# Kernel tuning notes

Measured on AMD Instinct MI355X. Metric: run time of the kernel, lower is better.

Reference implementation:

```python
import jax, jax.numpy as jnp
import numpy as np
import math

B, H, N, L = 8, 512, 64, 2048


def setup_inputs() -> dict:
    key = jax.random.key(0)
    k_u, k_c, k_dt, k_d, k_w, k_b, k_ar, k_ai = jax.random.split(key, 8)
    u = jax.random.normal(k_u, (B, H, L), dtype=jnp.float32)
    # C ~ complex randn, stored as (..., 2) real/imag pairs (torch.view_as_real)
    C_ri = jax.random.normal(k_c, (H, N, 2), dtype=jnp.float32)
    # log_dt ~ Uniform(log(dt_min), log(dt_max))
    lo, hi = math.log(0.001), math.log(0.1)
    log_dt = jax.random.uniform(k_dt, (H,), dtype=jnp.float32) * (hi - lo) + lo
    D = jax.random.normal(k_d, (H,), dtype=jnp.float32)
    # Conv1d(H, 2H, kernel_size=1) -> weight (2H, H), bias (2H), kaiming-ish scale
    W = jax.random.normal(k_w, (2 * H, H), dtype=jnp.float32) / math.sqrt(H)
    b = jax.random.normal(k_b, (2 * H,), dtype=jnp.float32) * 0.01
    # Fixed diagonal state matrix A: Re(A) uniform in [-0.9, -0.8), Im(A) random
    a_re = -0.9 + 0.1 * jax.random.uniform(k_ar, (N,), dtype=jnp.float32)
    a_im = math.pi * jnp.arange(N, dtype=jnp.float32)  # stable oscillation freqs
    A_ri = jnp.stack([a_re, a_im], axis=-1)
    return {"u": u, "C_ri": C_ri, "log_dt": log_dt, "D": D, "W": W, "b": b, "A_ri": A_ri}


def _forward(u, C_ri, log_dt, D, W, b, A_ri):
    Lseq = u.shape[-1]
    C = C_ri[..., 0] + 1j * C_ri[..., 1]          # (H, N) complex
    A = A_ri[..., 0] + 1j * A_ri[..., 1]          # (N,) complex
    dt = jnp.exp(log_dt)                           # (H,)
    dtA = dt[:, None] * A[None, :]                 # (H, N)
    # Vandermonde: exp(dtA * l) for l in [0, L)  -> (H, N, L) complex
    K = jnp.exp(dtA[:, :, None] * jnp.arange(Lseq, dtype=jnp.float32))
    Ct = C * (jnp.exp(dtA) - 1.0) / A              # (H, N)
    k = 2.0 * jnp.einsum('hn,hnl->hl', Ct, K).real  # (H, L) real kernel
    # FFT long convolution (linear conv via length-2L circular conv)
    nfft = 2 * Lseq
    y = jnp.fft.irfft(jnp.fft.rfft(u, n=nfft) * jnp.fft.rfft(k, n=nfft), n=nfft)[..., :Lseq]
    y = y + D[:, None] * u                         # skip connection
    y = jax.nn.gelu(y, approximate=False)          # torch nn.GELU default = exact erf
    # Conv1d kernel_size=1 == per-position linear, then GLU over channel dim
    z = jnp.einsum('oh,bhl->bol', W, y) + b[:, None]  # (B, 2H, L)
    a, g = jnp.split(z, 2, axis=-2)
    return a * jax.nn.sigmoid(g)                   # (B, H, L)


def reference(u, C_ri, log_dt, D, W, b, A_ri):
    return _forward(u, C_ri, log_dt, D, W, b, A_ri)
```

## Files before the change

### kernel.cpp

```cpp
#include <hip/hip_runtime.h>
#include <math.h>

#define Hh 512
#define Nn 64
#define Ll 2048
#define Bb 8

typedef float f32x4 __attribute__((ext_vector_type(4)));
typedef __bf16 bf16x8 __attribute__((ext_vector_type(8)));

__device__ __forceinline__ unsigned short f2b(float x) {
  unsigned u = __builtin_bit_cast(unsigned, x);
  u += 0x7FFFu + ((u >> 16) & 1u);
  return (unsigned short)(u >> 16);
}
__device__ __forceinline__ float b2f(unsigned short b) {
  unsigned u = ((unsigned)b) << 16;
  return __builtin_bit_cast(float, u);
}

union BF8 {
  unsigned short us[8];
  bf16x8 v;
  uint4 q;
};

__device__ __forceinline__ uint4 cvt8q(const float* p) {
  float4 a = *(const float4*)p;
  float4 b = *(const float4*)(p + 4);
  BF8 o;
  o.us[0] = f2b(a.x); o.us[1] = f2b(a.y); o.us[2] = f2b(a.z); o.us[3] = f2b(a.w);
  o.us[4] = f2b(b.x); o.us[5] = f2b(b.y); o.us[6] = f2b(b.z); o.us[7] = f2b(b.w);
  return o.q;
}

__device__ __forceinline__ float gelu_f(float y) {
  float t = y * y;
  float p = y * fmaf(0.0713548162726f, t, 1.59576912161f);
  float e = __expf(-p);
  return y / (1.0f + e);
}

__global__ __launch_bounds__(256) void prep_kernel(
    const float* __restrict__ C_ri, const float* __restrict__ log_dt,
    const float* __restrict__ A_ri, unsigned short* __restrict__ A1,
    unsigned short* __restrict__ A2, float* __restrict__ lamQ) {
  __shared__ char sm[49152];
  __shared__ float kqs[64];
  __shared__ float kpart[4][64];
  float* kt = (float*)sm;
  char* A1s = sm;
  char* A2s = sm + 16384;
  int h = blockIdx.x;
  int tid = threadIdx.x, n = tid & 63, part = tid >> 6;

  float dt = expf(log_dt[h]);
  float ar = A_ri[2 * n], ai = A_ri[2 * n + 1];
  float er = expf(dt * ar);
  float sn, cs;
  sincosf(dt * ai, &sn, &cs);
  float lr = er * cs, li = er * sn;
  float em1r = lr - 1.0f, em1i = li;
  float cr = C_ri[(h * 64 + n) * 2], ci = C_ri[(h * 64 + n) * 2 + 1];
  float numr = cr * em1r - ci * em1i;
  float numi = cr * em1i + ci * em1r;
  float den = ar * ar + ai * ai;
  float ctr = (numr * ar + numi * ai) / den;
  float cti = (numi * ar - numr * ai) / den;
  float l16r = lr, l16i = li;
#pragma unroll
  for (int s = 0; s < 4; ++s) {
    float t = l16r * l16r - l16i * l16i;
    l16i = 2.0f * l16r * l16i;
    l16r = t;
  }
  if (part == 0) {
    float qr = l16r, qi = l16i;
#pragma unroll
    for (int s = 0; s < 2; ++s) {
      float t = qr * qr - qi * qi;
      qi = 2.0f * qr * qi;
      qr = t;
    }
    lamQ[h * 128 + 2 * n] = qr;
    lamQ[h * 128 + 2 * n + 1] = qi;
  }
  float lpr = 1.0f, lpi = 0.0f;
  for (int s = 0; s < part; ++s) {
    float t = lpr * l16r - lpi * l16i;
    lpi = lpr * l16i + lpi * l16r;
    lpr = t;
  }
  int e0 = part * 16;
  {
    float vr = ctr * lpr - cti * lpi, vi = ctr * lpi + cti * lpr;
#pragma unroll
    for (int j = 0; j < 16; ++j) {
      kt[(e0 + j) * 64 + n] = vr;
      float t = vr * lr - vi * li;
      vi = vr * li + vi * lr;
      vr = t;
    }
  }
  __syncthreads();
  {
    float s = 0.0f;
#pragma unroll
    for (int j = 0; j < 16; ++j) s += kt[n * 64 + ((e0 + j + n) & 63)];
    kpart[part][n] = s;
  }
  __syncthreads();
  if (part == 0) kqs[n] = 2.0f * (kpart[0][n] + kpart[1][n] + kpart[2][n] + kpart[3][n]);
  __syncthreads();
  {
    BF8 R0, R1, I0, I1;
    float vr = lpr, vi = lpi;
#pragma unroll
    for (int j = 0; j < 16; ++j) {
      int idx = 15 - j;
      if (idx < 8) { R0.us[idx] = f2b(vr); I0.us[idx] = f2b(vi); }
      else         { R1.us[idx - 8] = f2b(vr); I1.us[idx - 8] = f2b(vi); }
      float t = vr * lr - vi * li;
      vi = vr * li + vi * lr;
      vr = t;
    }
    int qlo = 48 - e0;
    int rowR = 2 * n, rowI = 2 * n + 1;
    *(uint4*)(A1s + ((rowR * 128 + 2 * qlo) ^ ((rowR & 7) << 4))) = R0.q;
    *(uint4*)(A1s + ((rowR * 128 + 2 * qlo + 16) ^ ((rowR & 7) << 4))) = R1.q;
    *(uint4*)(A1s + ((rowI * 128 + 2 * qlo) ^ ((rowI & 7) << 4))) = I0.q;
    *(uint4*)(A1s + ((rowI * 128 + 2 * qlo + 16) ^ ((rowI & 7) << 4))) = I1.q;
  }
  {
    float c1r = ctr * lr - cti * li, c1i = ctr * li + cti * lr;
    float wr = 2.0f * (c1r * lpr - c1i * lpi);
    float wi = 2.0f * (c1r * lpi + c1i * lpr);
#pragma unroll
    for (int j = 0; j < 16; ++j) {
      int t = e0 + j;
      *(unsigned*)(A2s + ((t * 512 + 128 + 4 * n) ^ ((t & 7) << 4))) =
          (unsigned)f2b(wr) | ((unsigned)f2b(-wi) << 16);
      float tm = wr * lr - wi * li;
      wi = wr * li + wi * lr;
      wr = tm;
    }
  }
  {
    int tau = n;
#pragma unroll
    for (int half = 0; half < 2; ++half) {
      int q0 = e0 + half * 8;
      BF8 o;
#pragma unroll
      for (int j = 0; j < 8; ++j) {
        int q = q0 + j;
        o.us[j] = (q <= tau) ? f2b(kqs[tau - q]) : (unsigned short)0;
      }
      *(uint4*)(A2s + ((tau * 512 + 2 * q0) ^ ((tau & 7) << 4))) = o.q;
    }
  }
  __syncthreads();
#pragma unroll
  for (int i = 0; i < 4; ++i) {
    int byte = (i * 256 + tid) * 16;
    int row = byte >> 7;
    *(uint4*)((char*)A1 + (size_t)h * 16384 + byte) =
        *(const uint4*)(A1s + (byte ^ ((row & 7) << 4)));
  }
#pragma unroll
  for (int i = 0; i < 8; ++i) {
    int idx = i * 256 + tid;
    int row = idx >> 5;
    int byte = row * 512 + (idx & 31) * 16;
    *(uint4*)((char*)A2 + (size_t)h * 32768 + byte) =
        *(const uint4*)(A2s + (byte ^ ((row & 7) << 4)));
  }
}

__global__ __launch_bounds__(256) void wcvt_kernel(const float* __restrict__ W,
                                                   unsigned short* __restrict__ Wimg) {
  int id = blockIdx.x * 256 + threadIdx.x;
  int slot = id & 3, row = (id >> 2) & 127, kt = (id >> 9) & 15, ot = id >> 13;
  int o = (row < 64) ? (ot * 64 + row) : (512 + ot * 64 + row - 64);
  uint4 v = cvt8q(W + (size_t)o * 512 + kt * 32 + slot * 8);
  int sp = slot ^ ((row >> 1) & 3);
  *(uint4*)((char*)Wimg + (((size_t)ot * 16 + kt) * 8192) + row * 64 + sp * 16) = v;
}

__global__ __launch_bounds__(256, 5) void fused_conv_kernel(
    const float* __restrict__ u, const unsigned short* __restrict__ A1,
    const unsigned short* __restrict__ A2, const float* __restrict__ lamQ,
    const float* __restrict__ Dv, unsigned short* __restrict__ gy) {
  __shared__ char SXb[16384];
  __shared__ char Ub[8192];
  int h = blockIdx.x;
  int bs = blockIdx.y * 2;
  int tid = threadIdx.x;
  int w = tid >> 6, lane = tid & 63, lg = lane >> 4, l15 = lane & 15;

  {
    int row = tid >> 2, k0 = (tid & 3) * 16;
    int b = bs + (row >> 5), c = row & 31;
    const float* up = u + ((size_t)(b * Hh + h)) * Ll + c * 64 + k0;
    uint4 v0 = cvt8q(up), v1 = cvt8q(up + 8);
    int base = row * 128 + k0 * 2;
    int swz = (row & 7) << 4;
    *(uint4*)(Ub + (base ^ swz)) = v0;
    *(uint4*)(Ub + ((base + 16) ^ swz)) = v1;
  }
  bf16x8 a1f[2][2];
#pragma unroll
  for (int i = 0; i < 2; ++i) {
    int row = (2 * w + i) * 16 + l15;
#pragma unroll
    for (int kb = 0; kb < 2; ++kb)
      a1f[i][kb] = *(const bf16x8*)(A1 + ((size_t)h * 128 + row) * 64 + kb * 32 + lg * 8);
  }
  __syncthreads();

#pragma unroll
  for (int ct = 0; ct < 4; ++ct) {
    int bc = ct * 16 + l15;
    bf16x8 bu[2];
#pragma unroll
    for (int kb = 0; kb < 2; ++kb)
      bu[kb] = *(const bf16x8*)(Ub + ((bc * 128 + kb * 64 + lg * 16) ^ ((bc & 7) << 4)));
#pragma unroll
    for (int i = 0; i < 2; ++i) {
      f32x4 acc = {0.f, 0.f, 0.f, 0.f};
      acc = __builtin_amdgcn_mfma_f32_16x16x32_bf16(a1f[i][0], bu[0], acc, 0, 0, 0);
      acc = __builtin_amdgcn_mfma_f32_16x16x32_bf16(a1f[i][1], bu[1], acc, 0, 0, 0);
      int n2q = (2 * w + i) * 16 + lg * 4;
      uint2 pk;
      pk.x = f2b(acc[0]) | ((unsigned)f2b(acc[1]) << 16);
      pk.y = f2b(acc[2]) | ((unsigned)f2b(acc[3]) << 16);
      *(uint2*)(SXb + ((bc * 256 + n2q * 2) ^ ((bc & 7) << 4))) = pk;
    }
  }
  __syncthreads();

  {
    int nn = tid & 63, bloc = tid >> 6;
    if (bloc < 2) {
      float lqr = lamQ[h * 128 + 2 * nn], lqi = lamQ[h * 128 + 2 * nn + 1];
      float Xr = 0.f, Xi = 0.f;
      for (int c = 0; c < 32; ++c) {
        int bc = bloc * 32 + c;
        int byte = (bc * 256 + 4 * nn) ^ ((bc & 7) << 4);
        unsigned ps = *(const unsigned*)(SXb + byte);
        *(unsigned*)(SXb + byte) = (unsigned)f2b(Xr) | ((unsigned)f2b(Xi) << 16);
        float Sr = b2f((unsigned short)(ps & 0xFFFF));
        float Si = b2f((unsigned short)(ps >> 16));
        float nXr = lqr * Xr - lqi * Xi + Sr;
        float nXi = lqr * Xi + lqi * Xr + Si;
        Xr = nXr;
        Xi = nXi;
      }
    }
  }
  __syncthreads();

  bf16x8 a2f[6];
  int rowA = w * 16 + l15;
#pragma unroll
  for (int kb = 0; kb < 6; ++kb)
    a2f[kb] = *(const bf16x8*)(A2 + ((size_t)h * 64 + rowA) * 256 + kb * 32 + lg * 8);
  float Dh = Dv[h];
  int t0 = w * 16 + lg * 4;
  f32x4 acc4[4];
  uint2 usk[4];
#pragma unroll
  for (int ct = 0; ct < 4; ++ct) {
    int bc = ct * 16 + l15;
    f32x4 acc = {0.f, 0.f, 0.f, 0.f};
#pragma unroll
    for (int kb = 0; kb < 2; ++kb) {
      bf16x8 bu = *(const bf16x8*)(Ub + ((bc * 128 + kb * 64 + lg * 16) ^ ((bc & 7) << 4)));
      acc = __builtin_amdgcn_mfma_f32_16x16x32_bf16(a2f[kb], bu, acc, 0, 0, 0);
    }
#pragma unroll
    for (int kb = 2; kb < 6; ++kb) {
      bf16x8 bx = *(const bf16x8*)(SXb + ((bc * 256 + ((kb - 2) * 32 + lg * 8) * 2) ^ ((bc & 7) << 4)));
      acc = __builtin_amdgcn_mfma_f32_16x16x32_bf16(a2f[kb], bx, acc, 0, 0, 0);
    }
    acc4[ct] = acc;
    usk[ct] = *(const uint2*)(Ub + ((bc * 128 + t0 * 2) ^ ((bc & 7) << 4)));
  }
  __syncthreads();

#pragma unroll
  for (int ct = 0; ct < 4; ++ct) {
    int bc = ct * 16 + l15;
    const unsigned short* up = (const unsigned short*)&usk[ct];
    unsigned short e[4];
#pragma unroll
    for (int r = 0; r < 4; ++r) {
      float y = fmaf(Dh, b2f(up[r]), acc4[ct][r]);
      e[r] = f2b(gelu_f(y));
    }
    uint2 pk;
    pk.x = e[0] | ((unsigned)e[1] << 16);
    pk.y = e[2] | ((unsigned)e[3] << 16);
    *(uint2*)(Ub + ((bc * 128 + t0 * 2) ^ ((bc & 7) << 4))) = pk;
  }
  __syncthreads();

#pragma unroll
  for (int i = 0; i < 2; ++i) {
    int j = tid + 256 * i;
    int row = j >> 3, q = j & 7;
    int byte = row * 128 + q * 16;
    uint4 v = *(const uint4*)(Ub + (byte ^ ((row & 7) << 4)));
    int b = bs + (row >> 5), c = row & 31;
    *(uint4*)(gy + ((size_t)(b * Hh + h)) * Ll + c * 64 + q * 8) = v;
  }
}

__global__ __launch_bounds__(256, 3) void glu_kernel(
    const unsigned short* __restrict__ Wimg, const unsigned short* __restrict__ gy,
    const float* __restrict__ bias, float* __restrict__ out) {
  __shared__ char sA[2][8192];
  __shared__ char sB[2][8192];
  int lt = blockIdx.x;
  int ot = blockIdx.y;
  int b = lt >> 4, lseg = lt & 15;
  int t = threadIdx.x;
  int lane = t & 63, lg = lane >> 4, l15 = lane & 15;
  int w = t >> 6, wm = w >> 1, wn = w & 1;
  int p = t >> 4, cg = t & 15;
  const char* Abase = (const char*)Wimg + (size_t)ot * 131072;
  const unsigned short* gybase = gy + (size_t)b * Hh * Ll + lseg * 128 + cg * 8 + 2 * p * Ll;

  int offA[2], offG[2];
#pragma unroll
  for (int mt = 0; mt < 2; ++mt) {
    int rA = wm * 32 + mt * 16 + l15;
    offA[mt] = rA * 64 + ((lg ^ ((rA >> 1) & 3)) << 4);
    int rG = rA + 64;
    offG[mt] = rG * 64 + ((lg ^ ((rG >> 1) & 3)) << 4);
  }
  int offB[4];
#pragma unroll
  for (int nt = 0; nt < 4; ++nt) {
    int rB = wn * 64 + nt * 16 + l15;
    int pr = ((rB >> 3) << 3) | ((rB & 7) ^ ((rB >> 3) & 7));
    offB[nt] = (lg << 11) + (pr << 4);
  }
  int offW[8];
#pragma unroll
  for (int j = 0; j < 8; ++j) {
    int l = cg * 8 + j;
    int pr = (cg << 3) | (j ^ (cg & 7));
    offW[j] = ((p >> 2) << 11) + (pr << 4) + ((p & 3) << 2);
  }

  f32x4 accA[2][4], accG[2][4];
#pragma unroll
  for (int mt = 0; mt < 2; ++mt)
#pragma unroll
    for (int nt = 0; nt < 4; ++nt) {
      accA[mt][nt] = (f32x4){0.f, 0.f, 0.f, 0.f};
      accG[mt][nt] = (f32x4){0.f, 0.f, 0.f, 0.f};
    }

  {
    const char* ga = Abase + t * 16;
    __builtin_amdgcn_global_load_lds(ga, (char*)&sA[0][0] + t * 16, 16, 0, 0);
    __builtin_amdgcn_global_load_lds(ga + 4096, (char*)&sA[0][0] + 4096 + t * 16, 16, 0, 0);
    BF8 r0, r1;
    r0.q = *(const uint4*)gybase;
    r1.q = *(const uint4*)(gybase + Ll);
#pragma unroll
    for (int j = 0; j < 8; ++j)
      *(unsigned*)(&sB[0][0] + offW[j]) =
          (unsigned)r0.us[j] | ((unsigned)r1.us[j] << 16);
  }
  __syncthreads();

  for (int kt = 0; kt < 16; ++kt) {
    int cur = kt & 1;
    if (kt < 15) {
      const char* ga = Abase + (kt + 1) * 8192 + t * 16;
      char* da = (char*)&sA[cur ^ 1][0] + t * 16;
      __builtin_amdgcn_global_load_lds(ga, da, 16, 0, 0);
      __builtin_amdgcn_global_load_lds(ga + 4096, da + 4096, 16, 0, 0);
      BF8 r0, r1;
      r0.q = *(const uint4*)(gybase + (size_t)(kt + 1) * 32 * Ll);
      r1.q = *(const uint4*)(gybase + (size_t)(kt + 1) * 32 * Ll + Ll);
      char* db = &sB[cur ^ 1][0];
#pragma unroll
      for (int j = 0; j < 8; ++j)
        *(unsigned*)(db + offW[j]) =
            (unsigned)r0.us[j] | ((unsigned)r1.us[j] << 16);
    }
    const char* bufA = &sA[cur][0];
    const char* bufB = &sB[cur][0];
    bf16x8 aA[2], aG[2], bB[4];
#pragma unroll
    for (int mt = 0; mt < 2; ++mt) {
      aA[mt] = *(const bf16x8*)(bufA + offA[mt]);
      aG[mt] = *(const bf16x8*)(bufA + offG[mt]);
    }
#pragma unroll
    for (int nt = 0; nt < 4; ++nt)
      bB[nt] = *(const bf16x8*)(bufB + offB[nt]);
#pragma unroll
    for (int mt = 0; mt < 2; ++mt)
#pragma unroll
      for (int nt = 0; nt < 4; ++nt) {
        accA[mt][nt] = __builtin_amdgcn_mfma_f32_16x16x32_bf16(bB[nt], aA[mt], accA[mt][nt], 0, 0, 0);
        accG[mt][nt] = __builtin_amdgcn_mfma_f32_16x16x32_bf16(bB[nt], aG[mt], accG[mt][nt], 0, 0, 0);
      }
    __syncthreads();
  }

#pragma unroll
  for (int mt = 0; mt < 2; ++mt) {
    int oA = ot * 64 + wm * 32 + mt * 16 + l15;
    float ba = bias[oA];
    float bg = bias[512 + oA];
    float* orow = out + ((size_t)(b * Hh) + oA) * Ll + lseg * 128 + wn * 64 + lg * 4;
#pragma unroll
    for (int nt = 0; nt < 4; ++nt) {
      float4 res;
      float* rp = (float*)&res;
#pragma unroll
      for (int r = 0; r < 4; ++r) {
        float a = accA[mt][nt][r] + ba;
        float g = accG[mt][nt][r] + bg;
        rp[r] = a * (1.0f / (1.0f + __expf(-g)));
      }
      *(float4*)(orow + nt * 16) = res;
    }
  }
}

extern "C" void kernel_launch(void* const* d_in, const int* in_sizes, int n_in,
                              void* d_out, int out_size, void* d_ws,
                              size_t ws_size, hipStream_t stream) {
  const float* u      = (const float*)d_in[0];
  const float* C_ri   = (const float*)d_in[1];
  const float* log_dt = (const float*)d_in[2];
  const float* Dv     = (const float*)d_in[3];
  const float* W      = (const float*)d_in[4];
  const float* bias   = (const float*)d_in[5];
  const float* A_ri   = (const float*)d_in[6];
  float* out = (float*)d_out;

  char* ws = (char*)d_ws;
  unsigned short* A1   = (unsigned short*)ws;
  unsigned short* A2   = (unsigned short*)(ws + 8388608);
  float*          lamQ = (float*)(ws + 25165824);
  unsigned short* Wimg = (unsigned short*)(ws + 25427968);
  unsigned short* gy   = (unsigned short*)(ws + 26476544);

  prep_kernel<<<Hh, 256, 0, stream>>>(C_ri, log_dt, A_ri, A1, A2, lamQ);
  wcvt_kernel<<<256, 256, 0, stream>>>(W, Wimg);
  fused_conv_kernel<<<dim3(Hh, 4), 256, 0, stream>>>(u, A1, A2, lamQ, Dv, gy);
  glu_kernel<<<dim3(128, 8), 256, 0, stream>>>(Wimg, gy, bias, out);
}
```

Baseline: 62.89 us.

## Restructure GLU GEMM to keep activation tile resident and stream weights per wave

The GLU GEMM kernel now loads a full 512x64 activation tile into LDS once per block. Each wave then iterates over two output-channel tiles, streaming weight slices through a private double buffer with asynchronous global-to-LDS loads and explicit vmcnt waits, so block-wide barriers are gone from the K loop. This is meant to remove repeated activation reloads and per-iteration synchronisation. In exchange it uses about 128KB of LDS, allowing one block per CU, and launches only 256 blocks, which lowers occupancy and may leave CUs idle.

```diff
diff --git a/kernel.cpp b/kernel.cpp
--- a/kernel.cpp
+++ b/kernel.cpp
@@ -316,121 +316,124 @@
   }
 }
 
-__global__ __launch_bounds__(256, 3) void glu_kernel(
+__global__ __launch_bounds__(256, 1) void glu_kernel(
     const unsigned short* __restrict__ Wimg, const unsigned short* __restrict__ gy,
     const float* __restrict__ bias, float* __restrict__ out) {
-  __shared__ char sA[2][8192];
-  __shared__ char sB[2][8192];
-  int lt = blockIdx.x;
-  int ot = blockIdx.y;
-  int b = lt >> 4, lseg = lt & 15;
+  __shared__ char Bs[65536];
+  __shared__ char As[4][2][8192];
+  int lseg = blockIdx.x;
+  int b = blockIdx.y;
   int t = threadIdx.x;
   int lane = t & 63, lg = lane >> 4, l15 = lane & 15;
-  int w = t >> 6, wm = w >> 1, wn = w & 1;
-  int p = t >> 4, cg = t & 15;
-  const char* Abase = (const char*)Wimg + (size_t)ot * 131072;
-  const unsigned short* gybase = gy + (size_t)b * Hh * Ll + lseg * 128 + cg * 8 + 2 * p * Ll;
-
-  int offA[2], offG[2];
-#pragma unroll
-  for (int mt = 0; mt < 2; ++mt) {
-    int rA = wm * 32 + mt * 16 + l15;
+  int w = t >> 6;
+  int l0 = lseg * 64;
+  const char* Wbase = (const char*)Wimg;
+
+#pragma unroll
+  for (int d = 0; d < 2; ++d) {
+    const char* ga = Wbase + (size_t)(2 * w) * 131072 + d * 8192 + lane * 16;
+    char* da = &As[w][d][0] + lane * 16;
+#pragma unroll
+    for (int i = 0; i < 8; ++i)
+      __builtin_amdgcn_global_load_lds(ga + i * 1024, da + i * 1024, 16, 0, 0);
+  }
+
+  {
+    int p0 = t >> 3, cg = t & 7;
+#pragma unroll
+    for (int r = 0; r < 8; ++r) {
+      int P = r * 32 + p0;
+      const unsigned short* g = gy + ((size_t)(b * Hh + 2 * P)) * Ll + l0 + cg * 8;
+      BF8 r0, r1;
+      r0.q = *(const uint4*)g;
+      r1.q = *(const uint4*)(g + Ll);
+      int slot = P >> 2, word = P & 3;
+#pragma unroll
+      for (int j = 0; j < 8; ++j) {
+        int l = cg * 8 + j;
+        *(unsigned*)(Bs + l * 1024 + ((slot ^ l) << 4) + word * 4) =
+            (unsigned)r0.us[j] | ((unsigned)r1.us[j] << 16);
+      }
+    }
+  }
+  __syncthreads();
+
+  int offA[4], offG[4];
+#pragma unroll
+  for (int mt = 0; mt < 4; ++mt) {
+    int rA = mt * 16 + l15;
     offA[mt] = rA * 64 + ((lg ^ ((rA >> 1) & 3)) << 4);
     int rG = rA + 64;
     offG[mt] = rG * 64 + ((lg ^ ((rG >> 1) & 3)) << 4);
   }
-  int offB[4];
-#pragma unroll
-  for (int nt = 0; nt < 4; ++nt) {
-    int rB = wn * 64 + nt * 16 + l15;
-    int pr = ((rB >> 3) << 3) | ((rB & 7) ^ ((rB >> 3) & 7));
-    offB[nt] = (lg << 11) + (pr << 4);
-  }
-  int offW[8];
-#pragma unroll
-  for (int j = 0; j < 8; ++j) {
-    int l = cg * 8 + j;
-    int pr = (cg << 3) | (j ^ (cg & 7));
-    offW[j] = ((p >> 2) << 11) + (pr << 4) + ((p & 3) << 2);
-  }
-
-  f32x4 accA[2][4], accG[2][4];
-#pragma unroll
-  for (int mt = 0; mt < 2; ++mt)
-#pragma unroll
-    for (int nt = 0; nt < 4; ++nt) {
-      accA[mt][nt] = (f32x4){0.f, 0.f, 0.f, 0.f};
-      accG[mt][nt] = (f32x4){0.f, 0.f, 0.f, 0.f};
-    }
-
-  {
-    const char* ga = Abase + t * 16;
-    __builtin_amdgcn_global_load_lds(ga, (char*)&sA[0][0] + t * 16, 16, 0, 0);
-    __builtin_amdgcn_global_load_lds(ga + 4096, (char*)&sA[0][0] + 4096 + t * 16, 16, 0, 0);
-    BF8 r0, r1;
-    r0.q = *(const uint4*)gybase;
-    r1.q = *(const uint4*)(gybase + Ll);
-#pragma unroll
-    for (int j = 0; j < 8; ++j)
-      *(unsigned*)(&sB[0][0] + offW[j]) =
-          (unsigned)r0.us[j] | ((unsigned)r1.us[j] << 16);
-  }
-  __syncthreads();
-
-  for (int kt = 0; kt < 16; ++kt) {
-    int cur = kt & 1;
-    if (kt < 15) {
-      const char* ga = Abase + (kt + 1) * 8192 + t * 16;
-      char* da = (char*)&sA[cur ^ 1][0] + t * 16;
-      __builtin_amdgcn_global_load_lds(ga, da, 16, 0, 0);
-      __builtin_amdgcn_global_load_lds(ga + 4096, da + 4096, 16, 0, 0);
-      BF8 r0, r1;
-      r0.q = *(const uint4*)(gybase + (size_t)(kt + 1) * 32 * Ll);
-      r1.q = *(const uint4*)(gybase + (size_t)(kt + 1) * 32 * Ll + Ll);
-      char* db = &sB[cur ^ 1][0];
-#pragma unroll
-      for (int j = 0; j < 8; ++j)
-        *(unsigned*)(db + offW[j]) =
-            (unsigned)r0.us[j] | ((unsigned)r1.us[j] << 16);
-    }
-    const char* bufA = &sA[cur][0];
-    const char* bufB = &sB[cur][0];
-    bf16x8 aA[2], aG[2], bB[4];
-#pragma unroll
-    for (int mt = 0; mt < 2; ++mt) {
-      aA[mt] = *(const bf16x8*)(bufA + offA[mt]);
-      aG[mt] = *(const bf16x8*)(bufA + offG[mt]);
-    }
-#pragma unroll
-    for (int nt = 0; nt < 4; ++nt)
-      bB[nt] = *(const bf16x8*)(bufB + offB[nt]);
-#pragma unroll
-    for (int mt = 0; mt < 2; ++mt)
+
+#pragma unroll
+  for (int o2 = 0; o2 < 2; ++o2) {
+    int ot = 2 * w + o2;
+    f32x4 accA[4][4], accG[4][4];
+#pragma unroll
+    for (int mt = 0; mt < 4; ++mt)
 #pragma unroll
       for (int nt = 0; nt < 4; ++nt) {
-        accA[mt][nt] = __builtin_amdgcn_mfma_f32_16x16x32_bf16(bB[nt], aA[mt], accA[mt][nt], 0, 0, 0);
-        accG[mt][nt] = __builtin_amdgcn_mfma_f32_16x16x32_bf16(bB[nt], aG[mt], accG[mt][nt], 0, 0, 0);
-      }
-    __syncthreads();
-  }
-
-#pragma unroll
-  for (int mt = 0; mt < 2; ++mt) {
-    int oA = ot * 64 + wm * 32 + mt * 16 + l15;
-    float ba = bias[oA];
-    float bg = bias[512 + oA];
-    float* orow = out + ((size_t)(b * Hh) + oA) * Ll + lseg * 128 + wn * 64 + lg * 4;
-#pragma unroll
-    for (int nt = 0; nt < 4; ++nt) {
-      float4 res;
-      float* rp = (float*)&res;
-#pragma unroll
-      for (int r = 0; r < 4; ++r) {
-        float a = accA[mt][nt][r] + ba;
-        float g = accG[mt][nt][r] + bg;
-        rp[r] = a * (1.0f / (1.0f + __expf(-g)));
-      }
-      *(float4*)(orow + nt * 16) = res;
+        accA[mt][nt] = (f32x4){0.f, 0.f, 0.f, 0.f};
+        accG[mt][nt] = (f32x4){0.f, 0.f, 0.f, 0.f};
+      }
+    for (int kt = 0; kt < 16; ++kt) {
+      asm volatile("s_waitcnt vmcnt(8)" ::: "memory");
+      const char* bufA = &As[w][kt & 1][0];
+      bf16x8 aA[4], aG[4], bB[4];
+#pragma unroll
+      for (int mt = 0; mt < 4; ++mt) {
+        aA[mt] = *(const bf16x8*)(bufA + offA[mt]);
+        aG[mt] = *(const bf16x8*)(bufA + offG[mt]);
+      }
+#pragma unroll
+      for (int nt = 0; nt < 4; ++nt) {
+        int ll = nt * 16 + l15;
+        bB[nt] = *(const bf16x8*)(Bs + ll * 1024 + (((kt * 4 + lg) ^ ll) << 4));
+      }
+      __builtin_amdgcn_sched_barrier(0);
+      {
+        int pk = kt + 2, pot = ot, pvalid = 1;
+        if (pk >= 16) {
+          pk -= 16;
+          pot = ot + 1;
+          pvalid = (o2 == 0);
+        }
+        if (pvalid) {
+          const char* ga = Wbase + (size_t)pot * 131072 + pk * 8192 + lane * 16;
+          char* da = &As[w][kt & 1][0] + lane * 16;
+#pragma unroll
+          for (int i = 0; i < 8; ++i)
+            __builtin_amdgcn_global_load_lds(ga + i * 1024, da + i * 1024, 16, 0, 0);
+        }
+      }
+#pragma unroll
+      for (int mt = 0; mt < 4; ++mt)
+#pragma unroll
+        for (int nt = 0; nt < 4; ++nt) {
+          accA[mt][nt] = __builtin_amdgcn_mfma_f32_16x16x32_bf16(bB[nt], aA[mt], accA[mt][nt], 0, 0, 0);
+          accG[mt][nt] = __builtin_amdgcn_mfma_f32_16x16x32_bf16(bB[nt], aG[mt], accG[mt][nt], 0, 0, 0);
+        }
+    }
+#pragma unroll
+    for (int mt = 0; mt < 4; ++mt) {
+      int oA = ot * 64 + mt * 16 + l15;
+      float ba = bias[oA];
+      float bg = bias[512 + oA];
+      float* orow = out + ((size_t)(b * Hh) + oA) * Ll + l0 + lg * 4;
+#pragma unroll
+      for (int nt = 0; nt < 4; ++nt) {
+        float4 res;
+        float* rp = (float*)&res;
+#pragma unroll
+        for (int r = 0; r < 4; ++r) {
+          float a = accA[mt][nt][r] + ba;
+          float g = accG[mt][nt][r] + bg;
+          rp[r] = a * (1.0f / (1.0f + __expf(-g)));
+        }
+        *(float4*)(orow + nt * 16) = res;
+      }
     }
   }
 }
@@ -457,5 +460,5 @@
   prep_kernel<<<Hh, 256, 0, stream>>>(C_ri, log_dt, A_ri, A1, A2, lamQ);
   wcvt_kernel<<<256, 256, 0, stream>>>(W, Wimg);
   fused_conv_kernel<<<dim3(Hh, 4), 256, 0, stream>>>(u, A1, A2, lamQ, Dv, gy);
-  glu_kernel<<<dim3(128, 8), 256, 0, stream>>>(Wimg, gy, bias, out);
-}
+  glu_kernel<<<dim3(32, Bb), 256, 0, stream>>>(Wimg, gy, bias, out);
+}
```

Result: slower. 67.65 us (+7.6%).
